# Kernel tuning notes

Measured on AMD Instinct MI355X. Metric: run time of the kernel, lower is better.

The kernel has to match this reference:

```python
import jax, jax.numpy as jnp
import numpy as np

B, C, H, W = 4, 512, 64, 64
NUM_HEADS = 4
NUM_GROUPS = 32
EPS = 1e-5


def setup_inputs() -> dict:
    key = jax.random.key(0)
    ks = jax.random.split(key, 7)
    x = jax.random.normal(ks[0], (B, C, H, W), dtype=jnp.float32)
    gn_gamma = jnp.ones((C,), dtype=jnp.float32)
    gn_beta = jnp.zeros((C,), dtype=jnp.float32)
    # Conv2d 1x1 weights stored as [out_ch, in_ch]
    qkv_w = jax.random.normal(ks[1], (3 * C, C), dtype=jnp.float32) * (C ** -0.5)
    qkv_b = jax.random.normal(ks[2], (3 * C,), dtype=jnp.float32) * 0.01
    out_w = jax.random.normal(ks[3], (C, C), dtype=jnp.float32) * (C ** -0.5)
    out_b = jax.random.normal(ks[4], (C,), dtype=jnp.float32) * 0.01
    return {"x": x, "gn_gamma": gn_gamma, "gn_beta": gn_beta,
            "qkv_w": qkv_w, "qkv_b": qkv_b, "out_w": out_w, "out_b": out_b}


def _group_norm(x, gamma, beta):
    b, c, h, w = x.shape
    xg = x.reshape(b, NUM_GROUPS, c // NUM_GROUPS, h, w)
    mean = xg.mean(axis=(2, 3, 4), keepdims=True)
    var = xg.var(axis=(2, 3, 4), keepdims=True)
    xg = (xg - mean) * jax.lax.rsqrt(var + EPS)
    x = xg.reshape(b, c, h, w)
    return x * gamma[None, :, None, None] + beta[None, :, None, None]


def reference(x, gn_gamma, gn_beta, qkv_w, qkv_b, out_w, out_b):
    residual = x
    b, c, h, w = x.shape
    hc = c // NUM_HEADS
    n = h * w
    xn = _group_norm(x, gn_gamma, gn_beta)
    # 1x1 conv == channel matmul: [B, 3C, H, W]
    qkv = jnp.einsum('oc,bchw->bohw', qkv_w, xn) + qkv_b[None, :, None, None]
    q, k, v = jnp.split(qkv, 3, axis=1)
    # [B, C, H, W] -> [B, heads, N, hc]
    def to_heads(t):
        return t.reshape(b, NUM_HEADS, hc, n).transpose(0, 1, 3, 2)
    q, k, v = to_heads(q), to_heads(k), to_heads(v)
    scale = hc ** -0.5
    attn = jnp.einsum('bhnd,bhmd->bhnm', q, k) * scale
    attn = jax.nn.softmax(attn, axis=-1)
    o = jnp.einsum('bhnm,bhmd->bhnd', attn, v)
    # back to [B, C, H, W]
    o = o.transpose(0, 1, 3, 2).reshape(b, c, h, w)
    o = o + residual
    out = jnp.einsum('oc,bchw->bohw', out_w, o) + out_b[None, :, None, None]
    return out
```

## Files before the change

### kernel.cpp

```cpp
#include <hip/hip_runtime.h>
#include <math.h>

constexpr int BB = 4, CH = 512, NN = 4096, NHEADS = 4, NGROUPS = 32, HCH = 128;
constexpr float EPS = 1e-5f;
constexpr float SCALE = 0.08838834764831845f;
constexpr float LOG2E = 1.4426950408889634f;
constexpr float QSCALE = SCALE * LOG2E;
constexpr float THR = 11.541560327111707f;

typedef short bf16x8 __attribute__((ext_vector_type(8)));
typedef float f32x4 __attribute__((ext_vector_type(4)));
typedef float f32x16 __attribute__((ext_vector_type(16)));

__device__ __forceinline__ float bf2f(unsigned short u) {
    unsigned int x = ((unsigned int)u) << 16;
    float f; __builtin_memcpy(&f, &x, 4); return f;
}
__device__ __forceinline__ unsigned short f2bf(float f) {
    unsigned int x; __builtin_memcpy(&x, &f, 4);
    x += 0x7fff + ((x >> 16) & 1);
    return (unsigned short)(x >> 16);
}
__device__ __forceinline__ unsigned int cvtpk(float lo, float hi) {
    unsigned int r;
    asm("v_cvt_pk_bf16_f32 %0, %1, %2" : "=v"(r) : "v"(lo), "v"(hi));
    return r;
}
__device__ __forceinline__ float fexp2(float x) {
    float r; asm("v_exp_f32 %0, %1" : "=v"(r) : "v"(x)); return r;
}

__device__ __forceinline__ void gld16(const void* g, void* l) {
    __builtin_amdgcn_global_load_lds(
        (const __attribute__((address_space(1))) void*)g,
        (__attribute__((address_space(3))) void*)l, 16, 0, 0);
}

__global__ __launch_bounds__(256) void wconv_kernel(
    const float* __restrict__ qkv_w, const float* __restrict__ out_w,
    unsigned short* __restrict__ wq_bf, unsigned short* __restrict__ wo_bf,
    float* __restrict__ statsz)
{
    if (blockIdx.x == 0) statsz[threadIdx.x] = 0.f;
    int i4 = blockIdx.x * 256 + threadIdx.x;
    if (i4 < 196608) {
        float4 w = ((const float4*)qkv_w)[i4];
        int row = i4 >> 7;
        float sc = (row < 512) ? QSCALE : 1.0f;
        ushort4 o = { f2bf(w.x * sc), f2bf(w.y * sc), f2bf(w.z * sc), f2bf(w.w * sc) };
        *(ushort4*)&wq_bf[(size_t)i4 * 4] = o;
    } else {
        int j4 = i4 - 196608;
        float4 w = ((const float4*)out_w)[j4];
        ushort4 o = { f2bf(w.x), f2bf(w.y), f2bf(w.z), f2bf(w.w) };
        *(ushort4*)&wo_bf[(size_t)j4 * 4] = o;
    }
}

__global__ __launch_bounds__(256) void gn_stats_kernel(
    const float* __restrict__ x, float* __restrict__ stats)
{
    const int CPG = CH / NGROUPS;
    int bg = blockIdx.x >> 2, part = blockIdx.x & 3;
    int b = bg / NGROUPS, g = bg % NGROUPS;
    const size_t base = ((size_t)b * CH + (size_t)g * CPG) * NN
                      + (size_t)part * (CPG * NN / 4);
    const int total4 = CPG * NN / 16;
    int tid = threadIdx.x;

    const float4* x4 = (const float4*)(x + base);
    float sum = 0.f, sumsq = 0.f;
    for (int i = tid; i < total4; i += 256) {
        float4 v = x4[i];
        sum   += v.x + v.y + v.z + v.w;
        sumsq += v.x*v.x + v.y*v.y + v.z*v.z + v.w*v.w;
    }
    for (int off = 32; off > 0; off >>= 1) {
        sum   += __shfl_down(sum, off);
        sumsq += __shfl_down(sumsq, off);
    }
    __shared__ float s_sum[4], s_sq[4];
    int wid = tid >> 6, lane = tid & 63;
    if (lane == 0) { s_sum[wid] = sum; s_sq[wid] = sumsq; }
    __syncthreads();
    if (tid == 0) {
        float ts = 0.f, tq = 0.f;
        for (int i = 0; i < 4; i++) { ts += s_sum[i]; tq += s_sq[i]; }
        atomicAdd(&stats[bg * 2 + 0], ts);
        atomicAdd(&stats[bg * 2 + 1], tq);
    }
}

__global__ __launch_bounds__(256) void t1_kernel(
    const float* __restrict__ x, const float2* __restrict__ stats,
    const float* __restrict__ gamma, const float* __restrict__ beta,
    unsigned short* __restrict__ xnT, unsigned short* __restrict__ xT)
{
    __shared__ alignas(16) short Tn[64 * 80];
    __shared__ alignas(16) short Tr[64 * 80];
    int n0 = blockIdx.x * 64, c0 = blockIdx.y * 64, b = blockIdx.z;
    int tid = threadIdx.x;
    const float inv = 1.0f / 65536.0f;

    #pragma unroll
    for (int i = 0; i < 4; ++i) {
        int idx = tid + i * 256; int cl = idx >> 4, nq = idx & 15;
        int c = c0 + cl;
        float2 st = stats[b * NGROUPS + (c >> 4)];
        float mean = st.x * inv;
        float var  = st.y * inv - mean * mean;
        float rstd = rsqrtf(var + EPS);
        float gm = gamma[c], bt = beta[c];
        float4 f = *(const float4*)&x[((size_t)(b * CH + c)) * NN + n0 + nq * 4];
        float e0 = f.x, e1 = f.y, e2 = f.z, e3 = f.w;
        Tr[(nq * 4 + 0) * 80 + cl] = (short)f2bf(e0);
        Tr[(nq * 4 + 1) * 80 + cl] = (short)f2bf(e1);
        Tr[(nq * 4 + 2) * 80 + cl] = (short)f2bf(e2);
        Tr[(nq * 4 + 3) * 80 + cl] = (short)f2bf(e3);
        Tn[(nq * 4 + 0) * 80 + cl] = (short)f2bf((e0 - mean) * rstd * gm + bt);
        Tn[(nq * 4 + 1) * 80 + cl] = (short)f2bf((e1 - mean) * rstd * gm + bt);
        Tn[(nq * 4 + 2) * 80 + cl] = (short)f2bf((e2 - mean) * rstd * gm + bt);
        Tn[(nq * 4 + 3) * 80 + cl] = (short)f2bf((e3 - mean) * rstd * gm + bt);
    }
    __syncthreads();
    #pragma unroll
    for (int i = 0; i < 2; ++i) {
        int idx = tid + i * 256; int n = idx >> 3, ck = idx & 7;
        size_t gidx = ((size_t)(b * NN + n0 + n)) * CH + c0 + ck * 8;
        *(uint4*)&xnT[gidx] = *(uint4*)&Tn[n * 80 + ck * 8];
        *(uint4*)&xT[gidx]  = *(uint4*)&Tr[n * 80 + ck * 8];
    }
}

template<int MODE>
__global__ __launch_bounds__(256) void gemm_kernel(
    const unsigned short* __restrict__ A,
    const unsigned short* __restrict__ Bt,
    const float* __restrict__ bias,
    unsigned short* __restrict__ qT, unsigned short* __restrict__ kT,
    unsigned short* __restrict__ v, float* __restrict__ out)
{
    __shared__ alignas(16) short smem[2][2][128 * 64];
    short* Es = (short*)smem;
    float* Ef = (float*)smem;

    constexpr int GY = (MODE == 0) ? 12 : 4;
    int lin = blockIdx.x + 32 * (blockIdx.y + GY * blockIdx.z);
    constexpr int CPX = 32 * GY * 4 / 8;
    int wg = (lin & 7) * CPX + (lin >> 3);
    const int n0 = (wg % 32) * 128;
    const int m0 = ((wg / 32) % GY) * 128;
    const int b  = wg / (32 * GY);

    const int tid = threadIdx.x;
    const int wid = tid >> 6, l = tid & 63, lr = l & 15, lk = l >> 4;
    const int wm = (wid & 1) * 64, wn = (wid >> 1) * 64;
    const unsigned short* Bb = Bt + (size_t)b * NN * CH;

    int rr[4], LL[4], ch[4];
    #pragma unroll
    for (int i = 0; i < 4; ++i) {
        ch[i] = (wid * 4 + i) * 1024;
        int li = ch[i] + l * 16;
        int r = li >> 7, s = (li >> 4) & 7;
        rr[i] = r; LL[i] = s ^ (r & 7);
    }

    #define GSTAGE(buf, k0) do {                                                   \
        _Pragma("unroll")                                                          \
        for (int i = 0; i < 4; ++i) {                                              \
            gld16(&A [((size_t)(m0 + rr[i])) * CH + (k0) + LL[i] * 8],             \
                  (char*)&smem[buf][0][0] + ch[i]);                                \
            gld16(&Bb[((size_t)(n0 + rr[i])) * CH + (k0) + LL[i] * 8],             \
                  (char*)&smem[buf][1][0] + ch[i]);                                \
        }                                                                          \
    } while (0)

    f32x4 acc[4][4];
    #pragma unroll
    for (int i = 0; i < 4; ++i)
        #pragma unroll
        for (int j = 0; j < 4; ++j) acc[i][j] = (f32x4){0.f, 0.f, 0.f, 0.f};

    GSTAGE(0, 0);
    __syncthreads();

    int cur = 0;
    for (int ks = 0; ks < 8; ++ks) {
        if (ks < 7) GSTAGE(cur ^ 1, (ks + 1) * 64);
        const char* As = (const char*)&smem[cur][0][0];
        const char* Bs = (const char*)&smem[cur][1][0];
        #pragma unroll
        for (int kh = 0; kh < 2; ++kh) {
            const int sw = ((kh * 4 + lk) ^ (lr & 7)) << 4;
            bf16x8 af[4], bfr[4];
            #pragma unroll
            for (int t = 0; t < 4; ++t) {
                af[t]  = *(const bf16x8*)(As + (wm + t * 16 + lr) * 128 + sw);
                bfr[t] = *(const bf16x8*)(Bs + (wn + t * 16 + lr) * 128 + sw);
            }
            #pragma unroll
            for (int mt = 0; mt < 4; ++mt)
                #pragma unroll
                for (int nt = 0; nt < 4; ++nt)
                    acc[mt][nt] = __builtin_amdgcn_mfma_f32_16x16x32_bf16(
                        af[mt], bfr[nt], acc[mt][nt], 0, 0, 0);
        }
        __syncthreads();
        cur ^= 1;
    }
    #undef GSTAGE

    if (MODE == 0) {
        const bool isV = (m0 >= 1024);
        #pragma unroll
        for (int mt = 0; mt < 4; ++mt) {
            int mbase = m0 + wm + mt * 16 + lk * 4;
            int ml = wm + mt * 16 + lk * 4;
            float bsc = (m0 < 512) ? QSCALE : 1.0f;
            #pragma unroll
            for (int nt = 0; nt < 4; ++nt) {
                int nl = wn + nt * 16 + lr;
                f32x4 vv = acc[mt][nt];
                if (!isV) {
                    ushort4 o;
                    o.x = f2bf(vv[0] + bias[mbase + 0] * bsc);
                    o.y = f2bf(vv[1] + bias[mbase + 1] * bsc);
                    o.z = f2bf(vv[2] + bias[mbase + 2] * bsc);
                    o.w = f2bf(vv[3] + bias[mbase + 3] * bsc);
                    *(ushort4*)&Es[nl * 132 + ml] = o;
                } else {
                    #pragma unroll
                    for (int j = 0; j < 4; ++j)
                        Es[(ml + j) * 132 + nl] = (short)f2bf(vv[j] + bias[mbase + j]);
                }
            }
        }
        __syncthreads();
        int r16 = tid >> 4, c16 = tid & 15;
        if (!isV) {
            unsigned short* dst;
            if (m0 < 512) dst = qT + (((size_t)(b * 4 + (m0 >> 7))) * NN + n0) * 128;
            else          dst = kT + (((size_t)(b * 4 + ((m0 - 512) >> 7))) * NN + n0) * 128;
            #pragma unroll
            for (int p = 0; p < 8; ++p) {
                int nl = p * 16 + r16;
                uint4 w = *(const uint4*)&Es[nl * 132 + c16 * 8];
                *(uint4*)&dst[(size_t)nl * 128 + c16 * 8] = w;
            }
        } else {
            unsigned short* dst = v + ((size_t)(b * 512 + (m0 - 1024)) * NN) + n0;
            #pragma unroll
            for (int p = 0; p < 8; ++p) {
                int ml = p * 16 + r16;
                uint4 w = *(const uint4*)&Es[ml * 132 + c16 * 8];
                *(uint4*)&dst[(size_t)ml * NN + c16 * 8] = w;
            }
        }
    } else {
        for (int half = 0; half < 2; ++half) {
            __syncthreads();
            if ((wn >> 6) == half) {
                #pragma unroll
                for (int mt = 0; mt < 4; ++mt) {
                    int ml = wm + mt * 16 + lk * 4;
                    int mbase = m0 + ml;
                    #pragma unroll
                    for (int nt = 0; nt < 4; ++nt) {
                        int nl = nt * 16 + lr;
                        f32x4 vv = acc[mt][nt];
                        #pragma unroll
                        for (int j = 0; j < 4; ++j)
                            Ef[(ml + j) * 66 + nl] = vv[j] + bias[mbase + j];
                    }
                }
            }
            __syncthreads();
            #pragma unroll
            for (int i = 0; i < 8; ++i) {
                int idx = tid + i * 256;
                int r = idx >> 4, c4 = idx & 15;
                float4 w = *(const float4*)&Ef[r * 66 + c4 * 4];
                *(float4*)&out[((size_t)(b * CH + m0 + r)) * NN + n0 + half * 64 + c4 * 4] = w;
            }
        }
    }
}

__global__ __launch_bounds__(256, 2) void attn_kernel(
    const unsigned short* __restrict__ qT,
    const unsigned short* __restrict__ kT,
    const unsigned short* __restrict__ vg,
    const unsigned short* __restrict__ xT,
    unsigned short* __restrict__ aoT)
{
    __shared__ alignas(16) short Ks[2][64 * 128];
    __shared__ alignas(16) short Vs[2][64 * 128];

    int lin_id = blockIdx.x + 32 * (blockIdx.y + 4 * blockIdx.z);
    int wg = (lin_id & 7) * 64 + (lin_id >> 3);
    const int n0 = (wg & 31) * 128;
    const int h  = (wg >> 5) & 3;
    const int b  = wg >> 7;

    const int bh = b * 4 + h;
    const int tid = threadIdx.x, wid = tid >> 6, l = tid & 63;
    const int lq = l & 31, hi = l >> 5;
    const int wq0 = wid * 32;
    const int swz4 = (l & 15) << 4;
    const unsigned short* Qg = qT + (size_t)bh * NN * 128;
    const unsigned short* Kg = kT + (size_t)bh * NN * 128;
    const unsigned short* Vg = vg + (size_t)bh * 128 * NN;

    int kr[4], kc[4], vdd[4], vcc[4], ch[4];
    #pragma unroll
    for (int i = 0; i < 4; ++i) {
        ch[i] = (wid * 4 + i) * 1024;
        int li = ch[i] + l * 16;
        int r = li >> 8, s = (li >> 4) & 15;
        int L = s ^ (r & 15);
        kr[i] = r; kc[i] = L;
        vdd[i] = r + 64 * (L >> 3);
        vcc[i] = L & 7;
    }

    #define STAGE(buf, m0k) do {                                                   \
        _Pragma("unroll")                                                          \
        for (int i = 0; i < 4; ++i) {                                              \
            gld16(&Kg[(size_t)((m0k) + kr[i]) * 128 + kc[i] * 8],                  \
                  (char*)&Ks[buf][0] + ch[i]);                                     \
            gld16(&Vg[(size_t)vdd[i] * NN + (m0k) + vcc[i] * 8],                   \
                  (char*)&Vs[buf][0] + ch[i]);                                     \
        }                                                                          \
    } while (0)

    STAGE(0, 0);

    bf16x8 qr[8];
    #pragma unroll
    for (int dk = 0; dk < 8; ++dk)
        qr[dk] = *(const bf16x8*)&Qg[((size_t)(n0 + wq0 + lq)) * 128 + dk * 16 + hi * 8];

    f32x16 ov[4];
    #pragma unroll
    for (int dt = 0; dt < 4; ++dt)
        #pragma unroll
        for (int r = 0; r < 16; ++r) ov[dt][r] = 0.f;
    float mrun = -1e30f, lrun = 0.f;

    __syncthreads();

    int cur = 0;
    for (int t = 0; t < 64; ++t) {
        if (t < 63) STAGE(cur ^ 1, (t + 1) * 64);

        const char* Kc = (const char*)&Ks[cur][0];
        const char* Vc = (const char*)&Vs[cur][0];

        f32x16 s0, s1;
        #pragma unroll
        for (int r = 0; r < 16; ++r) { s0[r] = 0.f; s1[r] = 0.f; }
        __builtin_amdgcn_s_setprio(1);
        #pragma unroll
        for (int dk = 0; dk < 8; ++dk) {
            bf16x8 k0 = *(const bf16x8*)(Kc + (lq)      * 256 + ((dk * 32 + hi * 16) ^ swz4));
            bf16x8 k1 = *(const bf16x8*)(Kc + (32 + lq) * 256 + ((dk * 32 + hi * 16) ^ swz4));
            s0 = __builtin_amdgcn_mfma_f32_32x32x16_bf16(k0, qr[dk], s0, 0, 0, 0);
            s1 = __builtin_amdgcn_mfma_f32_32x32x16_bf16(k1, qr[dk], s1, 0, 0, 0);
        }
        __builtin_amdgcn_s_setprio(0);

        float m8[8];
        #pragma unroll
        for (int r = 0; r < 8; ++r)
            m8[r] = fmaxf(fmaxf(s0[r], s0[r + 8]), fmaxf(s1[r], s1[r + 8]));
        float t0 = fmaxf(fmaxf(m8[0], m8[1]), m8[2]);
        float t1_ = fmaxf(fmaxf(m8[3], m8[4]), m8[5]);
        float t2 = fmaxf(fmaxf(m8[6], m8[7]), t0);
        float pm = fmaxf(t1_, t2);
        pm = fmaxf(pm, __shfl_xor(pm, 32));

        int defer = (pm - mrun) <= THR;
        if (!__all(defer)) {
            float mnew = fmaxf(mrun, pm);
            float corr = fexp2(mrun - mnew);
            lrun *= corr; mrun = mnew;
            #pragma unroll
            for (int dt = 0; dt < 4; ++dt)
                #pragma unroll
                for (int r = 0; r < 16; ++r) ov[dt][r] *= corr;
        }
        float ps = 0.f;
        #pragma unroll
        for (int r = 0; r < 16; ++r) { float e = fexp2(s0[r] - mrun); s0[r] = e; ps += e; }
        #pragma unroll
        for (int r = 0; r < 16; ++r) { float e = fexp2(s1[r] - mrun); s1[r] = e; ps += e; }
        ps += __shfl_xor(ps, 32);
        lrun += ps;

        unsigned int u0[8], u1[8];
        #pragma unroll
        for (int m = 0; m < 8; ++m) {
            u0[m] = cvtpk(s0[2 * m], s0[2 * m + 1]);
            u1[m] = cvtpk(s1[2 * m], s1[2 * m + 1]);
        }
        bf16x8 pf[4];
        #pragma unroll
        for (int kt = 0; kt < 2; ++kt)
            #pragma unroll
            for (int hh = 0; hh < 2; ++hh) {
                const unsigned int* u = kt ? u1 : u0;
                unsigned int w0 = u[4*hh + 0], w2 = u[4*hh + 2];
                unsigned int w1 = u[4*hh + 1], w3 = u[4*hh + 3];
                asm("v_permlane32_swap_b32 %0, %1" : "+v"(w0), "+v"(w2));
                asm("v_permlane32_swap_b32 %0, %1" : "+v"(w1), "+v"(w3));
                unsigned int w[4] = { w0, w1, w2, w3 };
                bf16x8 p; __builtin_memcpy(&p, w, 16);
                pf[kt * 2 + hh] = p;
            }

        __builtin_amdgcn_s_setprio(1);
        #pragma unroll
        for (int dt = 0; dt < 4; ++dt)
            #pragma unroll
            for (int kt2 = 0; kt2 < 4; ++kt2) {
                bf16x8 vf = *(const bf16x8*)(Vc + ((dt & 1) * 32 + lq) * 256 +
                                             ((((dt >> 1) * 8 + kt2 * 2 + hi) << 4) ^ swz4));
                ov[dt] = __builtin_amdgcn_mfma_f32_32x32x16_bf16(vf, pf[kt2], ov[dt], 0, 0, 0);
            }
        __builtin_amdgcn_s_setprio(0);

        __syncthreads();
        cur ^= 1;
    }
    #undef STAGE

    float linv = 1.0f / lrun;
    const int n = n0 + wq0 + lq;
    #pragma unroll
    for (int dt = 0; dt < 4; ++dt)
        #pragma unroll
        for (int m = 0; m < 4; ++m) {
            int d = dt * 32 + m * 8 + hi * 4;
            size_t gidx = ((size_t)(b * NN + n)) * CH + h * 128 + d;
            unsigned short xv[4];
            *(ushort4*)xv = *(const ushort4*)&xT[gidx];
            unsigned int w0 = cvtpk(ov[dt][4*m + 0] * linv + bf2f(xv[0]),
                                    ov[dt][4*m + 1] * linv + bf2f(xv[1]));
            unsigned int w1 = cvtpk(ov[dt][4*m + 2] * linv + bf2f(xv[2]),
                                    ov[dt][4*m + 3] * linv + bf2f(xv[3]));
            unsigned long long wv = (unsigned long long)w0 |
                                    ((unsigned long long)w1 << 32);
            *(unsigned long long*)&aoT[gidx] = wv;
        }
}

extern "C" void kernel_launch(void* const* d_in, const int* in_sizes, int n_in,
                              void* d_out, int out_size, void* d_ws, size_t ws_size,
                              hipStream_t stream) {
    const float* x      = (const float*)d_in[0];
    const float* gamma  = (const float*)d_in[1];
    const float* beta   = (const float*)d_in[2];
    const float* qkv_w  = (const float*)d_in[3];
    const float* qkv_b  = (const float*)d_in[4];
    const float* out_w  = (const float*)d_in[5];
    const float* out_b  = (const float*)d_in[6];
    float* out = (float*)d_out;

    char* ws = (char*)d_ws;
    const size_t SZ = (size_t)BB * CH * NN * 2;
    unsigned short* xnT   = (unsigned short*)(ws);
    unsigned short* xT    = (unsigned short*)(ws + SZ);
    unsigned short* qT    = (unsigned short*)(ws + 2 * SZ);
    unsigned short* kT    = (unsigned short*)(ws + 3 * SZ);
    unsigned short* vbuf  = (unsigned short*)(ws + 4 * SZ);
    unsigned short* aoT   = (unsigned short*)(ws + 5 * SZ);
    unsigned short* wq_bf = (unsigned short*)(ws + 6 * SZ);
    unsigned short* wo_bf = (unsigned short*)(ws + 6 * SZ + (size_t)1536 * 512 * 2);
    float* stats = (float*)(ws + 6 * SZ + (size_t)2048 * 512 * 2);

    wconv_kernel<<<dim3(1024), 256, 0, stream>>>(qkv_w, out_w, wq_bf, wo_bf, stats);
    gn_stats_kernel<<<dim3(BB * NGROUPS * 4), 256, 0, stream>>>(x, stats);
    t1_kernel<<<dim3(NN / 64, CH / 64, BB), 256, 0, stream>>>(
        x, (const float2*)stats, gamma, beta, xnT, xT);
    gemm_kernel<0><<<dim3(NN / 128, 1536 / 128, BB), 256, 0, stream>>>(
        wq_bf, xnT, qkv_b, qT, kT, vbuf, nullptr);
    attn_kernel<<<dim3(NN / 128, NHEADS, BB), 256, 0, stream>>>(qT, kT, vbuf, xT, aoT);
    gemm_kernel<1><<<dim3(NN / 128, CH / 128, BB), 256, 0, stream>>>(
        wo_bf, aoT, out_b, nullptr, nullptr, nullptr, out);
}
```

Baseline: 259.1 us.

## Merge prep kernels and compute softmax row sums with a ones-vector MFMA

Combines the weight-conversion kernel and the group-norm statistics kernel into one launch, and zeroes the stats buffer with a memset instead. In the attention loop, the per-row softmax denominator is no longer summed on the VALU with a cross-lane shuffle. It is accumulated by an extra MFMA against a vector of bf16 ones, with the same rescaling as the output. This moves work off the VALU onto the matrix unit at the cost of extra MFMAs and an accumulator register set, and the sum now comes from bf16-rounded probabilities.

After: 260.4 us. No clear change (+0.5%).

```diff
diff --git a/kernel.cpp b/kernel.cpp
--- a/kernel.cpp
+++ b/kernel.cpp
@@ -36,32 +36,32 @@
         (__attribute__((address_space(3))) void*)l, 16, 0, 0);
 }
 
-__global__ __launch_bounds__(256) void wconv_kernel(
+__global__ __launch_bounds__(256) void prep_kernel(
     const float* __restrict__ qkv_w, const float* __restrict__ out_w,
+    const float* __restrict__ x,
     unsigned short* __restrict__ wq_bf, unsigned short* __restrict__ wo_bf,
-    float* __restrict__ statsz)
+    float* __restrict__ stats)
 {
-    if (blockIdx.x == 0) statsz[threadIdx.x] = 0.f;
-    int i4 = blockIdx.x * 256 + threadIdx.x;
-    if (i4 < 196608) {
-        float4 w = ((const float4*)qkv_w)[i4];
-        int row = i4 >> 7;
-        float sc = (row < 512) ? QSCALE : 1.0f;
-        ushort4 o = { f2bf(w.x * sc), f2bf(w.y * sc), f2bf(w.z * sc), f2bf(w.w * sc) };
-        *(ushort4*)&wq_bf[(size_t)i4 * 4] = o;
-    } else {
-        int j4 = i4 - 196608;
-        float4 w = ((const float4*)out_w)[j4];
-        ushort4 o = { f2bf(w.x), f2bf(w.y), f2bf(w.z), f2bf(w.w) };
-        *(ushort4*)&wo_bf[(size_t)j4 * 4] = o;
-    }
-}
-
-__global__ __launch_bounds__(256) void gn_stats_kernel(
-    const float* __restrict__ x, float* __restrict__ stats)
-{
+    int bid = blockIdx.x;
+    if (bid < 1024) {
+        int i4 = bid * 256 + threadIdx.x;
+        if (i4 < 196608) {
+            float4 w = ((const float4*)qkv_w)[i4];
+            int row = i4 >> 7;
+            float sc = (row < 512) ? QSCALE : 1.0f;
+            ushort4 o = { f2bf(w.x * sc), f2bf(w.y * sc), f2bf(w.z * sc), f2bf(w.w * sc) };
+            *(ushort4*)&wq_bf[(size_t)i4 * 4] = o;
+        } else {
+            int j4 = i4 - 196608;
+            float4 w = ((const float4*)out_w)[j4];
+            ushort4 o = { f2bf(w.x), f2bf(w.y), f2bf(w.z), f2bf(w.w) };
+            *(ushort4*)&wo_bf[(size_t)j4 * 4] = o;
+        }
+        return;
+    }
     const int CPG = CH / NGROUPS;
-    int bg = blockIdx.x >> 2, part = blockIdx.x & 3;
+    int gb = bid - 1024;
+    int bg = gb >> 2, part = gb & 3;
     int b = bg / NGROUPS, g = bg % NGROUPS;
     const size_t base = ((size_t)b * CH + (size_t)g * CPG) * NN
                       + (size_t)part * (CPG * NN / 4);
@@ -341,12 +341,18 @@
     for (int dk = 0; dk < 8; ++dk)
         qr[dk] = *(const bf16x8*)&Qg[((size_t)(n0 + wq0 + lq)) * 128 + dk * 16 + hi * 8];
 
-    f32x16 ov[4];
+    bf16x8 vone;
+    #pragma unroll
+    for (int j = 0; j < 8; ++j) vone[j] = (short)0x3F80;
+
+    f32x16 ov[4], ovs;
     #pragma unroll
     for (int dt = 0; dt < 4; ++dt)
         #pragma unroll
         for (int r = 0; r < 16; ++r) ov[dt][r] = 0.f;
-    float mrun = -1e30f, lrun = 0.f;
+    #pragma unroll
+    for (int r = 0; r < 16; ++r) ovs[r] = 0.f;
+    float mrun = -1e30f;
 
     __syncthreads();
 
@@ -384,19 +390,18 @@
         if (!__all(defer)) {
             float mnew = fmaxf(mrun, pm);
             float corr = fexp2(mrun - mnew);
-            lrun *= corr; mrun = mnew;
+            mrun = mnew;
             #pragma unroll
             for (int dt = 0; dt < 4; ++dt)
                 #pragma unroll
                 for (int r = 0; r < 16; ++r) ov[dt][r] *= corr;
-        }
-        float ps = 0.f;
-        #pragma unroll
-        for (int r = 0; r < 16; ++r) { float e = fexp2(s0[r] - mrun); s0[r] = e; ps += e; }
-        #pragma unroll
-        for (int r = 0; r < 16; ++r) { float e = fexp2(s1[r] - mrun); s1[r] = e; ps += e; }
-        ps += __shfl_xor(ps, 32);
-        lrun += ps;
+            #pragma unroll
+            for (int r = 0; r < 16; ++r) ovs[r] *= corr;
+        }
+        #pragma unroll
+        for (int r = 0; r < 16; ++r) s0[r] = fexp2(s0[r] - mrun);
+        #pragma unroll
+        for (int r = 0; r < 16; ++r) s1[r] = fexp2(s1[r] - mrun);
 
         unsigned int u0[8], u1[8];
         #pragma unroll
@@ -428,6 +433,9 @@
                                              ((((dt >> 1) * 8 + kt2 * 2 + hi) << 4) ^ swz4));
                 ov[dt] = __builtin_amdgcn_mfma_f32_32x32x16_bf16(vf, pf[kt2], ov[dt], 0, 0, 0);
             }
+        #pragma unroll
+        for (int kt2 = 0; kt2 < 4; ++kt2)
+            ovs = __builtin_amdgcn_mfma_f32_32x32x16_bf16(vone, pf[kt2], ovs, 0, 0, 0);
         __builtin_amdgcn_s_setprio(0);
 
         __syncthreads();
@@ -435,7 +443,7 @@
     }
     #undef STAGE
 
-    float linv = 1.0f / lrun;
+    float linv = 1.0f / ovs[0];
     const int n = n0 + wq0 + lq;
     #pragma unroll
     for (int dt = 0; dt < 4; ++dt)
@@ -479,8 +487,8 @@
     unsigned short* wo_bf = (unsigned short*)(ws + 6 * SZ + (size_t)1536 * 512 * 2);
     float* stats = (float*)(ws + 6 * SZ + (size_t)2048 * 512 * 2);
 
-    wconv_kernel<<<dim3(1024), 256, 0, stream>>>(qkv_w, out_w, wq_bf, wo_bf, stats);
-    gn_stats_kernel<<<dim3(BB * NGROUPS * 4), 256, 0, stream>>>(x, stats);
+    hipMemsetAsync(stats, 0, 256 * sizeof(float), stream);
+    prep_kernel<<<dim3(1536), 256, 0, stream>>>(qkv_w, out_w, x, wq_bf, wo_bf, stats);
     t1_kernel<<<dim3(NN / 64, CH / 64, BB), 256, 0, stream>>>(
         x, (const float2*)stats, gamma, beta, xnT, xT);
     gemm_kernel<0><<<dim3(NN / 128, 1536 / 128, BB), 256, 0, stream>>>(
```
